# Performance work log

Hardware: AMD Instinct MI355X
Metric: run time of the kernel (lower is better)

Reference implementation:

```python
import jax, jax.numpy as jnp
import numpy as np

STOCH = 32; DETER = 512; OBS = 64; ACT = 8; HID = 512
B = 1024; T = 64
MIN_STD = 0.1; UPD_BIAS = -1.0; LN_EPS = 1e-3


def _ln(x, g, b):
    # LayerNorm(eps=0.001), biased variance as in torch
    m = jnp.mean(x, axis=-1, keepdims=True)
    v = jnp.mean((x - m) ** 2, axis=-1, keepdims=True)
    return (x - m) / jnp.sqrt(v + LN_EPS) * g + b


def setup_inputs() -> dict:
    key = jax.random.key(0)
    ks = jax.random.split(key, 12)
    def rn(k, shape, scale=0.05):
        return jax.random.normal(k, shape, jnp.float32) * scale
    return {
        "obs": jax.random.normal(ks[0], (B, T, OBS), jnp.float32),
        "action": jax.random.normal(ks[1], (B, T, ACT), jnp.float32),
        "is_first": jax.random.randint(ks[2], (B, T), 0, 2, jnp.int32),
        # prior_in: Linear(stoch+act -> hidden, no bias) + LN
        "W_pi": rn(ks[3], (STOCH + ACT, HID)), "g_pi": jnp.ones(HID), "b_pi": jnp.zeros(HID),
        # GRUCell: Linear(hidden+deter -> 3*deter, no bias) + LN
        "W_gru": rn(ks[4], (HID + DETER, 3 * DETER)), "g_gru": jnp.ones(3 * DETER), "b_gru": jnp.zeros(3 * DETER),
        # prior_out: Linear(deter -> hidden, no bias) + LN
        "W_po": rn(ks[5], (DETER, HID)), "g_po": jnp.ones(HID), "b_po": jnp.zeros(HID),
        # prior_stats: Linear(hidden -> 2*stoch)
        "W_ps": rn(ks[6], (HID, 2 * STOCH)), "b_ps": jnp.zeros(2 * STOCH),
        # post_net: Linear(deter+obs -> hidden, no bias) + LN
        "W_pn": rn(ks[7], (DETER + OBS, HID)), "g_pn": jnp.ones(HID), "b_pn": jnp.zeros(HID),
        # post_stats: Linear(hidden -> 2*stoch)
        "W_pt": rn(ks[8], (HID, 2 * STOCH)), "b_pt": jnp.zeros(2 * STOCH),
        # learned initial deterministic state (1, deter)
        "init_deter": rn(ks[9], (1, DETER), 0.1),
    }


def reference(obs, action, is_first,
              W_pi, g_pi, b_pi, W_gru, g_gru, b_gru, W_po, g_po, b_po,
              W_ps, b_ps, W_pn, g_pn, b_pn, W_pt, b_pt, init_deter):
    silu = jax.nn.silu
    Bsz = obs.shape[0]
    # initial_state: deter = tanh(learned), stoch = prior mean at that deter
    d_init = jnp.tanh(init_deter)  # (1, DETER)
    h0 = silu(_ln(d_init @ W_po, g_po, b_po))
    s_init = (h0 @ W_ps + b_ps)[..., :STOCH]  # prior mean
    d_init = jnp.broadcast_to(d_init, (Bsz, DETER))
    s_init = jnp.broadcast_to(s_init, (Bsz, STOCH))

    def step(carry, inp):
        deter, stoch = carry
        obs_t, act_t, first_t = inp  # (B,OBS),(B,ACT),(B,)
        m = (first_t > 0)[:, None]
        deter = jnp.where(m, d_init, deter)
        stoch = jnp.where(m, s_init, stoch)
        act_t = jnp.where(m, 0.0, act_t)
        # prior / img step
        x = silu(_ln(jnp.concatenate([stoch, act_t], -1) @ W_pi, g_pi, b_pi))
        gates = _ln(jnp.concatenate([x, deter], -1) @ W_gru, g_gru, b_gru)
        r, c, u = jnp.split(gates, 3, -1)
        r = jax.nn.sigmoid(r)
        u = jax.nn.sigmoid(u + UPD_BIAS)
        cand = silu(r * c)
        deter_n = u * cand + (1.0 - u) * deter
        hp = silu(_ln(deter_n @ W_po, g_po, b_po))
        ps = hp @ W_ps + b_ps
        p_mean, p_raw = jnp.split(ps, 2, -1)
        p_std = jax.nn.softplus(p_raw) + MIN_STD
        # posterior
        hq = silu(_ln(jnp.concatenate([deter_n, obs_t], -1) @ W_pn, g_pn, b_pn))
        qs = hq @ W_pt + b_pt
        q_mean, q_raw = jnp.split(qs, 2, -1)
        q_std = jax.nn.softplus(q_raw) + MIN_STD
        stoch_n = q_mean  # deterministic (mode) rollout for reproducibility
        out = jnp.concatenate([q_mean, q_std, stoch_n, p_mean, p_std, deter_n], -1)
        return (deter_n, stoch_n), out

    xs = (jnp.swapaxes(obs, 0, 1), jnp.swapaxes(action, 0, 1), jnp.swapaxes(is_first, 0, 1))
    _, outs = jax.lax.scan(step, (d_init, s_init), xs)  # (T,B,5*STOCH+DETER)
    return jnp.swapaxes(outs, 0, 1)  # (B,T,672)
```

## Files before the change

### kernel.cpp

```cpp
#include <hip/hip_runtime.h>
#include <hip/hip_bf16.h>
#include <math.h>

#define BB 1024
#define TT 64
#define OBSN 64
#define ACTN 8
#define STOCHN 32
#define DETERN 512
#define HIDN 512
#define G3N 1536
#define CATPI 40
#define OUTC 672
#define LNEPS 1e-3f
#define MINSTD 0.1f
#define UPDBIAS -1.0f

typedef __attribute__((ext_vector_type(8))) short short8;
typedef __attribute__((ext_vector_type(4))) float f32x4;

__device__ __forceinline__ float sigmoidf_(float x) { return 1.f / (1.f + expf(-x)); }
__device__ __forceinline__ float siluf_(float x) { return x / (1.f + expf(-x)); }
__device__ __forceinline__ float softplusf_(float x) { return (x > 20.f) ? x : log1pf(expf(x)); }

__device__ __forceinline__ float b2f(short u) {
    unsigned x = ((unsigned)(unsigned short)u) << 16;
    return __builtin_bit_cast(float, x);
}
__device__ __forceinline__ short f2b(float f) {
    __hip_bfloat16 h = __float2bfloat16(f);
    return __builtin_bit_cast(short, h);
}

__device__ __forceinline__ f32x4 mfma16(short8 a, short8 b, f32x4 c) {
    return __builtin_amdgcn_mfma_f32_16x16x32_bf16(a, b, c, 0, 0, 0);
}

__device__ __forceinline__ void gload_lds16(const void* g, void* l) {
    __builtin_amdgcn_global_load_lds((const __attribute__((address_space(1))) void*)g,
                                     (__attribute__((address_space(3))) void*)l, 16, 0, 0);
}

__device__ __forceinline__ void wred2(float& a, float& b) {
#pragma unroll
    for (int off = 32; off; off >>= 1) {
        a += __shfl_xor(a, off);
        b += __shfl_xor(b, off);
    }
}

__device__ __forceinline__ short8 frag_ld(const short* base, int row, int ks, int lk) {
    int slot = (ks * 4 + lk) ^ (row & 7);
    return *(const short8*)((const char*)base + row * 1024 + (slot << 4));
}
__device__ __forceinline__ short8 frag_ld64(const short* base, int row, int ks, int lk) {
    int slot = ((ks * 4 + lk) ^ (row & 7)) & 7;
    return *(const short8*)((const char*)base + row * 128 + (slot << 4));
}

template <int NFC, int AMT>
__device__ __forceinline__ void stage_tile(const __hip_bfloat16* A0, int ld0, int K0, const __hip_bfloat16* A1,
                                           int ld1, const __hip_bfloat16* Wt, int ldW, int wn0, int cm0, int k0,
                                           char* smA, char* smB) {
    int tid = threadIdx.x, wid = tid >> 6, lane = tid & 63;
    int rseg = lane >> 3, slot = lane & 7;
    const __hip_bfloat16* Ab;
    int ldA, kloc;
    if (k0 < K0) {
        Ab = A0; ldA = ld0; kloc = k0;
    } else {
        Ab = A1; ldA = ld1; kloc = k0 - K0;
    }
#pragma unroll
    for (int i = 0; i < AMT; ++i) {
        int seg = wid * AMT + i;
        int row = seg * 8 + rseg;
        int kk = kloc + ((slot ^ (row & 7)) << 3);
        gload_lds16(Ab + (size_t)(cm0 + row) * ldA + kk, smA + seg * 1024);
    }
#pragma unroll
    for (int i = 0; i < NFC; ++i) {
        int seg = wid * NFC + i;
        int row = seg * 8 + rseg;
        int kk = k0 + ((slot ^ (row & 7)) << 3);
        gload_lds16(Wt + (size_t)(wn0 + row) * ldW + kk, smB + seg * 1024);
    }
}

template <int NFC, int AMT>
__device__ __forceinline__ void compute_tile(const char* smA, const char* smB, f32x4 (&acc)[AMT][NFC]) {
    int lane = threadIdx.x & 63, wid = threadIdx.x >> 6;
    int wr = wid >> 1, wc = wid & 1;
#pragma unroll
    for (int ks = 0; ks < 2; ++ks) {
        short8 af[AMT], bfr[NFC];
        int kslot = ks * 4 + (lane >> 4);
#pragma unroll
        for (int m = 0; m < AMT; ++m) {
            int row = wr * (16 * AMT) + m * 16 + (lane & 15);
            af[m] = *(const short8*)(smA + row * 128 + ((kslot ^ (row & 7)) << 4));
        }
#pragma unroll
        for (int n = 0; n < NFC; ++n) {
            int row = wc * (16 * NFC) + n * 16 + (lane & 15);
            bfr[n] = *(const short8*)(smB + row * 128 + ((kslot ^ (row & 7)) << 4));
        }
#pragma unroll
        for (int m = 0; m < AMT; ++m)
#pragma unroll
            for (int n = 0; n < NFC; ++n) acc[m][n] = mfma16(af[m], bfr[n], acc[m][n]);
    }
}

template <int NFC, int AMT>
__device__ __forceinline__ void gemm_tile_db(const __hip_bfloat16* A0, int ld0, int K0, const __hip_bfloat16* A1,
                                             int ld1, const __hip_bfloat16* Wt, int ldW, int wn0, float* C, int ldc,
                                             int cm0, int cn0, int nK, char* smem) {
    char* smA[2] = {smem, smem + AMT * 4096};
    char* smB[2] = {smem + 2 * AMT * 4096, smem + 2 * AMT * 4096 + NFC * 4096};
    f32x4 acc[AMT][NFC] = {};
    stage_tile<NFC, AMT>(A0, ld0, K0, A1, ld1, Wt, ldW, wn0, cm0, 0, smA[0], smB[0]);
    for (int kt = 0; kt < nK; ++kt) {
        if (kt + 1 < nK) {
            stage_tile<NFC, AMT>(A0, ld0, K0, A1, ld1, Wt, ldW, wn0, cm0, (kt + 1) * 64, smA[(kt + 1) & 1],
                                 smB[(kt + 1) & 1]);
            constexpr int NL = NFC + AMT;
            if constexpr (NL == 5) asm volatile("s_waitcnt vmcnt(5)" ::: "memory");
            else if constexpr (NL == 4) asm volatile("s_waitcnt vmcnt(4)" ::: "memory");
            else asm volatile("s_waitcnt vmcnt(3)" ::: "memory");
        } else {
            asm volatile("s_waitcnt vmcnt(0)" ::: "memory");
        }
        __builtin_amdgcn_s_barrier();
        compute_tile<NFC, AMT>(smA[kt & 1], smB[kt & 1], acc);
        __builtin_amdgcn_s_barrier();
    }
    int lane = threadIdx.x & 63, wid = threadIdx.x >> 6;
    int wr = wid >> 1, wc = wid & 1;
    int r0 = cm0 + wr * (16 * AMT) + ((lane >> 4) << 2);
    int c0 = cn0 + wc * 16 * NFC + (lane & 15);
#pragma unroll
    for (int m = 0; m < AMT; ++m)
#pragma unroll
        for (int n = 0; n < NFC; ++n)
#pragma unroll
            for (int i = 0; i < 4; ++i)
                C[(size_t)(r0 + m * 16 + i) * ldc + c0 + n * 16] = acc[m][n][i];
}

__global__ __launch_bounds__(256) void k_gemm_gru(const __hip_bfloat16* __restrict__ xbf,
                                                  const __hip_bfloat16* __restrict__ dbf,
                                                  const __hip_bfloat16* __restrict__ WgT,
                                                  float* __restrict__ gates) {
    __shared__ __align__(16) char smem[32768];
    int bm = blockIdx.x & 31, bn = blockIdx.x >> 5;
    gemm_tile_db<3, 1>(xbf, 512, 512, dbf, 512, WgT, 1024, bn * 96, gates, G3N, bm * 32, bn * 96, 16, smem);
}

__global__ __launch_bounds__(256) void k_update(int t, const float* __restrict__ gates,
                                                const float* __restrict__ g_gru, const float* __restrict__ b_gru,
                                                float* __restrict__ deter, __hip_bfloat16* __restrict__ dbf,
                                                float* __restrict__ out) {
    const int tid = threadIdx.x;
    const int prow = tid >> 6, l = tid & 63;
    const int gr = blockIdx.x * 4 + prow;
    const int j0 = l * 8;
    const float* gp = gates + (size_t)gr * G3N;
    float g0[8], g1[8], g2[8];
    float s = 0.f, q = 0.f;
#pragma unroll
    for (int e = 0; e < 8; e += 4) {
        f32x4 a = *(const f32x4*)(gp + j0 + e);
        f32x4 b = *(const f32x4*)(gp + 512 + j0 + e);
        f32x4 c = *(const f32x4*)(gp + 1024 + j0 + e);
#pragma unroll
        for (int u = 0; u < 4; ++u) {
            g0[e + u] = a[u];
            g1[e + u] = b[u];
            g2[e + u] = c[u];
            s += a[u] + b[u] + c[u];
            q += a[u] * a[u] + b[u] * b[u] + c[u] * c[u];
        }
    }
    wred2(s, q);
    float m = s * (1.f / 1536.f), iv = rsqrtf(q * (1.f / 1536.f) - m * m + LNEPS);
    float dn[8];
    float* dp = deter + (size_t)gr * 512 + j0;
#pragma unroll
    for (int e = 0; e < 8; e += 4) {
        f32x4 dv = *(const f32x4*)(dp + e);
#pragma unroll
        for (int u = 0; u < 4; ++u) {
            int col = j0 + e + u;
            float rv = sigmoidf_((g0[e + u] - m) * iv * g_gru[col] + b_gru[col]);
            float cv = (g1[e + u] - m) * iv * g_gru[512 + col] + b_gru[512 + col];
            float uv = sigmoidf_((g2[e + u] - m) * iv * g_gru[1024 + col] + b_gru[1024 + col] + UPDBIAS);
            dn[e + u] = uv * siluf_(rv * cv) + (1.f - uv) * dv[u];
        }
    }
    size_t ob = ((size_t)gr * TT + t) * OUTC + 160 + j0;
    short8 h;
#pragma unroll
    for (int e = 0; e < 8; e += 4) {
        *(f32x4*)(dp + e) = *(const f32x4*)&dn[e];
        *(f32x4*)(out + ob + e) = *(const f32x4*)&dn[e];
    }
#pragma unroll
    for (int u = 0; u < 8; ++u) h[u] = f2b(dn[u]);
    *(short8*)(dbf + (size_t)gr * 512 + j0) = h;
}

__global__ __launch_bounds__(256) void k_gemm_hq(int t, const __hip_bfloat16* __restrict__ dbf,
                                                 const __hip_bfloat16* __restrict__ obsbf,
                                                 const __hip_bfloat16* __restrict__ WpnT,
                                                 float* __restrict__ hq_raw) {
    __shared__ __align__(16) char smem[24576];
    int bm = blockIdx.x & 31, bn = blockIdx.x >> 5;
    gemm_tile_db<2, 1>(dbf, 512, 512, obsbf + (size_t)t * OBSN, TT * OBSN, WpnT, 576, bn * 64, hq_raw, 512,
                       bm * 32, bn * 64, 9, smem);
}

__global__ __launch_bounds__(256) void k_finish(int t, const float* __restrict__ hq_raw,
                                                const float* __restrict__ g_pn, const float* __restrict__ b_pn,
                                                const __hip_bfloat16* __restrict__ WptT,
                                                const float* __restrict__ b_pt, const int* __restrict__ isf,
                                                const float* __restrict__ action, const float* __restrict__ dinit,
                                                const float* __restrict__ sinit, float* __restrict__ deter,
                                                __hip_bfloat16* __restrict__ dbf,
                                                const __hip_bfloat16* __restrict__ Wpibf,
                                                const float* __restrict__ g_pi, const float* __restrict__ b_pi,
                                                __hip_bfloat16* __restrict__ xbf, float* __restrict__ out) {
    __shared__ float hql[4][512];
    __shared__ float a_ls[4][40];
    const int wid = threadIdx.x >> 6, l = threadIdx.x & 63;
    const int gr = blockIdx.x * 4 + wid;
    const int j0 = l * 8;
    const float* hr = hq_raw + (size_t)gr * 512;
    float h[8];
    *(f32x4*)&h[0] = *(const f32x4*)(hr + j0);
    *(f32x4*)&h[4] = *(const f32x4*)(hr + j0 + 4);
    float s = 0.f, q = 0.f;
#pragma unroll
    for (int e = 0; e < 8; ++e) {
        s += h[e];
        q += h[e] * h[e];
    }
    wred2(s, q);
    float m = s * (1.f / 512.f), iv = rsqrtf(q * (1.f / 512.f) - m * m + LNEPS);
#pragma unroll
    for (int e = 0; e < 8; ++e) h[e] = siluf_((h[e] - m) * iv * g_pn[j0 + e] + b_pn[j0 + e]);
    *(f32x4*)&hql[wid][j0] = *(const f32x4*)&h[0];
    *(f32x4*)&hql[wid][j0 + 4] = *(const f32x4*)&h[4];
    __syncthreads();
    float acc = b_pt[l];
    const __hip_bfloat16* wr = WptT + (size_t)l * 512;
    const float* hq = hql[wid];
#pragma unroll 4
    for (int k0 = 0; k0 < 512; k0 += 8) {
        short8 w = *(const short8*)(wr + k0);
        f32x4 a0 = *(const f32x4*)(hq + k0);
        f32x4 a1 = *(const f32x4*)(hq + k0 + 4);
#pragma unroll
        for (int e = 0; e < 4; ++e) {
            acc += b2f(w[e]) * a0[e];
            acc += b2f(w[4 + e]) * a1[e];
        }
    }
    size_t ob = ((size_t)gr * TT + t) * OUTC;
    if (l < 32) {
        out[ob + l] = acc;
        out[ob + 64 + l] = acc;
    } else {
        out[ob + 32 + (l - 32)] = softplusf_(acc) + MINSTD;
    }
    if (t + 1 >= TT) return;
    int f1 = isf[(size_t)gr * TT + t + 1] > 0;
    if (l < 32)
        a_ls[wid][l] = f1 ? sinit[l] : acc;
    else if (l < 40)
        a_ls[wid][l] = f1 ? 0.f : action[((size_t)gr * TT + t + 1) * ACTN + (l - 32)];
    if (f1) {
        f32x4 d0 = *(const f32x4*)(dinit + j0);
        f32x4 d1 = *(const f32x4*)(dinit + j0 + 4);
        *(f32x4*)(deter + (size_t)gr * 512 + j0) = d0;
        *(f32x4*)(deter + (size_t)gr * 512 + j0 + 4) = d1;
        short8 db;
#pragma unroll
        for (int e = 0; e < 4; ++e) {
            db[e] = f2b(d0[e]);
            db[4 + e] = f2b(d1[e]);
        }
        *(short8*)(dbf + (size_t)gr * 512 + j0) = db;
    }
    __syncthreads();
    float o[8] = {};
    const float* a_s = a_ls[wid];
    for (int k = 0; k < CATPI; ++k) {
        float a = a_s[k];
        short8 w = *(const short8*)(Wpibf + k * 512 + j0);
#pragma unroll
        for (int e = 0; e < 8; ++e) o[e] += a * b2f(w[e]);
    }
    float s2 = 0.f, q2 = 0.f;
#pragma unroll
    for (int e = 0; e < 8; ++e) {
        s2 += o[e];
        q2 += o[e] * o[e];
    }
    wred2(s2, q2);
    float m2 = s2 * (1.f / 512.f), iv2 = rsqrtf(q2 * (1.f / 512.f) - m2 * m2 + LNEPS);
    short8 xo;
#pragma unroll
    for (int e = 0; e < 8; ++e) xo[e] = f2b(siluf_((o[e] - m2) * iv2 * g_pi[j0 + e] + b_pi[j0 + e]));
    *(short8*)(xbf + (size_t)gr * 512 + j0) = xo;
}

__global__ __launch_bounds__(512) void k_post_p(const float* __restrict__ outr,
                                                const __hip_bfloat16* __restrict__ WpoT,
                                                const float* __restrict__ g_po, const float* __restrict__ b_po,
                                                const __hip_bfloat16* __restrict__ WpsT,
                                                const float* __restrict__ b_ps, float* __restrict__ out) {
    __shared__ short Abuf[64 * 512];
    __shared__ __align__(16) short Wbuf[512 * 64];
    __shared__ float red[8 * 64 * 2];
    __shared__ float redc[64 * 2];
    const int tid = threadIdx.x, wid = tid >> 6, lane = tid & 63, lr = lane & 15, lk = lane >> 4;
    const int base = blockIdx.x * 64;
    const int c0 = wid * 64 + lr;

#pragma unroll
    for (int it = 0; it < 8; ++it) {
        int idx = it * 512 + tid;
        int row = idx >> 6, slot = idx & 63;
        int k = (slot ^ (row & 7)) << 3;
        const float* src = outr + ((size_t)(base + row) * OUTC + 160 + k);
        f32x4 a = *(const f32x4*)src;
        f32x4 bb = *(const f32x4*)(src + 4);
        short8 v;
#pragma unroll
        for (int e = 0; e < 4; ++e) {
            v[e] = f2b(a[e]);
            v[4 + e] = f2b(bb[e]);
        }
        *(short8*)((char*)Abuf + idx * 16) = v;
    }
    auto stageW = [&](int ck) {
#pragma unroll
        for (int i = 0; i < 8; ++i) {
            int seg = wid * 8 + i;
            int row = seg * 8 + (lane >> 3);
            int kk = ck * 64 + (((lane & 7) ^ (row & 7)) << 3);
            gload_lds16(WpoT + (size_t)row * 512 + kk, (char*)Wbuf + seg * 1024);
        }
    };
    __syncthreads();
    f32x4 acc[4][4] = {};
    for (int ck = 0; ck < 8; ++ck) {
        stageW(ck);
        asm volatile("s_waitcnt vmcnt(0)" ::: "memory");
        __builtin_amdgcn_s_barrier();
#pragma unroll
        for (int ks = 0; ks < 2; ++ks) {
            short8 af[4];
#pragma unroll
            for (int rt = 0; rt < 4; ++rt) af[rt] = frag_ld(Abuf, rt * 16 + lr, ck * 2 + ks, lk);
#pragma unroll
            for (int f = 0; f < 4; ++f) {
                short8 bf = frag_ld64(Wbuf, c0 + f * 16, ks, lk);
#pragma unroll
                for (int rt = 0; rt < 4; ++rt) acc[rt][f] = mfma16(af[rt], bf, acc[rt][f]);
            }
        }
        __builtin_amdgcn_s_barrier();
    }
#pragma unroll
    for (int qq = 0; qq < 8; ++qq) {
        int sI = qq * 512 + tid;
        int row = sI >> 6, slot = sI & 63;
        int k = (slot ^ (row & 7)) << 3;
        gload_lds16(WpsT + (size_t)row * 512 + k, (char*)Abuf + (qq * 512 + wid * 64) * 16);
    }
    {
        float s[4][4], q[4][4];
#pragma unroll
        for (int rt = 0; rt < 4; ++rt)
#pragma unroll
            for (int i = 0; i < 4; ++i) {
                float ss = 0.f, qq2 = 0.f;
#pragma unroll
                for (int f = 0; f < 4; ++f) {
                    float v = acc[rt][f][i];
                    ss += v;
                    qq2 += v * v;
                }
                s[rt][i] = ss;
                q[rt][i] = qq2;
            }
#pragma unroll
        for (int msk = 1; msk <= 8; msk <<= 1)
#pragma unroll
            for (int rt = 0; rt < 4; ++rt)
#pragma unroll
                for (int i = 0; i < 4; ++i) {
                    s[rt][i] += __shfl_xor(s[rt][i], msk);
                    q[rt][i] += __shfl_xor(q[rt][i], msk);
                }
        if (lr == 0)
#pragma unroll
            for (int rt = 0; rt < 4; ++rt)
#pragma unroll
                for (int i = 0; i < 4; ++i) {
                    int row = rt * 16 + lk * 4 + i;
                    red[(wid * 64 + row) * 2 + 0] = s[rt][i];
                    red[(wid * 64 + row) * 2 + 1] = q[rt][i];
                }
        __syncthreads();
        if (tid < 128) {
            int row = tid >> 1, v = tid & 1;
            float a = 0.f;
#pragma unroll
            for (int w = 0; w < 8; ++w) a += red[(w * 64 + row) * 2 + v];
            redc[row * 2 + v] = a;
        }
        __syncthreads();
#pragma unroll
        for (int rt = 0; rt < 4; ++rt)
#pragma unroll
            for (int i = 0; i < 4; ++i) {
                int row = rt * 16 + lk * 4 + i;
                float mm = redc[row * 2] * (1.f / 512.f);
                float vv = redc[row * 2 + 1] * (1.f / 512.f) - mm * mm;
                float ivv = rsqrtf(vv + LNEPS);
#pragma unroll
                for (int f = 0; f < 4; ++f) {
                    int col = c0 + f * 16;
                    float v = siluf_((acc[rt][f][i] - mm) * ivv * g_po[col] + b_po[col]);
                    *(short*)((char*)Wbuf + row * 1024 +
                              ((((col >> 3) ^ (row & 7)) << 4) | ((col & 7) << 1))) = f2b(v);
                }
            }
    }
    asm volatile("s_waitcnt vmcnt(0)" ::: "memory");
    __syncthreads();
    if (wid < 4) {
        int col = wid * 16 + lr;
        f32x4 ap[4] = {};
#pragma unroll 2
        for (int ks = 0; ks < 16; ++ks) {
            short8 bfr = frag_ld(Abuf, col, ks, lk);
#pragma unroll
            for (int rt = 0; rt < 4; ++rt) {
                short8 a = frag_ld(Wbuf, rt * 16 + lr, ks, lk);
                ap[rt] = mfma16(a, bfr, ap[rt]);
            }
        }
        float bias = b_ps[col];
#pragma unroll
        for (int rt = 0; rt < 4; ++rt)
#pragma unroll
            for (int i = 0; i < 4; ++i) {
                int gidx = base + rt * 16 + lk * 4 + i;
                float v = ap[rt][i] + bias;
                if (col < 32)
                    out[(size_t)gidx * OUTC + 96 + col] = v;
                else
                    out[(size_t)gidx * OUTC + 128 + (col - 32)] = softplusf_(v) + MINSTD;
            }
    }
}

__global__ __launch_bounds__(256) void k_prior0(const int* __restrict__ isf, const float* __restrict__ action,
                                                const float* __restrict__ dinit, const float* __restrict__ sinit,
                                                const __hip_bfloat16* __restrict__ Wpibf,
                                                const float* __restrict__ g_pi, const float* __restrict__ b_pi,
                                                float* __restrict__ deter0, __hip_bfloat16* __restrict__ dbf,
                                                __hip_bfloat16* __restrict__ xbf) {
    __shared__ float a_ls[4][40];
    const int wid = threadIdx.x >> 6, l = threadIdx.x & 63;
    const int gr = blockIdx.x * 4 + wid;
    const int j0 = l * 8;
    int f0 = isf[(size_t)gr * TT] > 0;
    if (l < 32)
        a_ls[wid][l] = sinit[l];
    else if (l < 40)
        a_ls[wid][l] = f0 ? 0.f : action[(size_t)gr * TT * ACTN + (l - 32)];
    f32x4 d0 = *(const f32x4*)(dinit + j0);
    f32x4 d1 = *(const f32x4*)(dinit + j0 + 4);
    *(f32x4*)(deter0 + (size_t)gr * 512 + j0) = d0;
    *(f32x4*)(deter0 + (size_t)gr * 512 + j0 + 4) = d1;
    short8 db;
#pragma unroll
    for (int e = 0; e < 4; ++e) {
        db[e] = f2b(d0[e]);
        db[4 + e] = f2b(d1[e]);
    }
    *(short8*)(dbf + (size_t)gr * 512 + j0) = db;
    __syncthreads();
    float o[8] = {};
    const float* a_s = a_ls[wid];
    for (int k = 0; k < CATPI; ++k) {
        float a = a_s[k];
        short8 w = *(const short8*)(Wpibf + k * 512 + j0);
#pragma unroll
        for (int e = 0; e < 8; ++e) o[e] += a * b2f(w[e]);
    }
    float s2 = 0.f, q2 = 0.f;
#pragma unroll
    for (int e = 0; e < 8; ++e) {
        s2 += o[e];
        q2 += o[e] * o[e];
    }
    wred2(s2, q2);
    float m2 = s2 * (1.f / 512.f), iv2 = rsqrtf(q2 * (1.f / 512.f) - m2 * m2 + LNEPS);
    short8 xo;
#pragma unroll
    for (int e = 0; e < 8; ++e) xo[e] = f2b(siluf_((o[e] - m2) * iv2 * g_pi[j0 + e] + b_pi[j0 + e]));
    *(short8*)(xbf + (size_t)gr * 512 + j0) = xo;
}

template <int NV>
__device__ __forceinline__ void breduce(float* v, float* red, int nwaves) {
    __syncthreads();
#pragma unroll
    for (int off = 32; off > 0; off >>= 1)
#pragma unroll
        for (int q = 0; q < NV; ++q) v[q] += __shfl_down(v[q], off);
    int lane = threadIdx.x & 63, w = threadIdx.x >> 6;
    if (lane == 0)
        for (int q = 0; q < NV; ++q) red[w * NV + q] = v[q];
    __syncthreads();
    if ((int)threadIdx.x < NV) {
        float s = 0.f;
        for (int ww = 0; ww < nwaves; ++ww) s += red[ww * NV + threadIdx.x];
        red[nwaves * NV + threadIdx.x] = s;
    }
    __syncthreads();
#pragma unroll
    for (int q = 0; q < NV; ++q) v[q] = red[nwaves * NV + q];
}

__global__ __launch_bounds__(512) void k_init(const float* __restrict__ init_deter, const float* __restrict__ W_po,
                                              const float* __restrict__ g_po, const float* __restrict__ b_po,
                                              const float* __restrict__ W_ps, const float* __restrict__ b_ps,
                                              float* __restrict__ dinit, float* __restrict__ sinit) {
    __shared__ float d_s[512], h_s[512], red[40];
    int tid = threadIdx.x;
    float dv = tanhf(init_deter[tid]);
    d_s[tid] = dv;
    dinit[tid] = dv;
    __syncthreads();
    float acc = 0.f;
    for (int k = 0; k < 512; ++k) acc += d_s[k] * W_po[k * 512 + tid];
    float v[2] = {acc, acc * acc};
    breduce<2>(v, red, 8);
    float m = v[0] / 512.f, va = v[1] / 512.f - m * m, iv = rsqrtf(va + LNEPS);
    h_s[tid] = siluf_((acc - m) * iv * g_po[tid] + b_po[tid]);
    __syncthreads();
    if (tid < 32) {
        float s = b_ps[tid];
        for (int k = 0; k < 512; ++k) s += h_s[k] * W_ps[k * 64 + tid];
        sinit[tid] = s;
    }
}

__global__ __launch_bounds__(256) void k_transpose_bf(const float* __restrict__ src,
                                                      __hip_bfloat16* __restrict__ dst, int K, int N) {
    __shared__ float tle[32][33];
    int nTK = K >> 5;
    int k0 = (blockIdx.x % nTK) * 32;
    int n0 = (blockIdx.x / nTK) * 32;
    int tx = threadIdx.x & 31, ty = threadIdx.x >> 5;
#pragma unroll
    for (int i = 0; i < 4; ++i) tle[ty + i * 8][tx] = src[(size_t)(k0 + ty + i * 8) * N + n0 + tx];
    __syncthreads();
#pragma unroll
    for (int i = 0; i < 4; ++i)
        dst[(size_t)(n0 + ty + i * 8) * K + k0 + tx] = __float2bfloat16(tle[tx][ty + i * 8]);
}

__global__ __launch_bounds__(256) void k_cvt_bf(const float* __restrict__ src, __hip_bfloat16* __restrict__ dst,
                                                int n) {
    for (int i = blockIdx.x * 256 + threadIdx.x; i < n; i += gridDim.x * 256) dst[i] = __float2bfloat16(src[i]);
}

extern "C" void kernel_launch(void* const* d_in, const int* in_sizes, int n_in, void* d_out, int out_size, void* d_ws,
                              size_t ws_size, hipStream_t stream) {
    const float* obs = (const float*)d_in[0];
    const float* action = (const float*)d_in[1];
    const int* is_first = (const int*)d_in[2];
    const float* W_pi = (const float*)d_in[3];
    const float* g_pi = (const float*)d_in[4];
    const float* b_pi = (const float*)d_in[5];
    const float* W_gru = (const float*)d_in[6];
    const float* g_gru = (const float*)d_in[7];
    const float* b_gru = (const float*)d_in[8];
    const float* W_po = (const float*)d_in[9];
    const float* g_po = (const float*)d_in[10];
    const float* b_po = (const float*)d_in[11];
    const float* W_ps = (const float*)d_in[12];
    const float* b_ps = (const float*)d_in[13];
    const float* W_pn = (const float*)d_in[14];
    const float* g_pn = (const float*)d_in[15];
    const float* b_pn = (const float*)d_in[16];
    const float* W_pt = (const float*)d_in[17];
    const float* b_pt = (const float*)d_in[18];
    const float* init_deter = (const float*)d_in[19];
    float* out = (float*)d_out;

    char* p = (char*)d_ws;
    auto alloc = [&](size_t bytes) {
        char* r = p;
        p += (bytes + 255) & ~(size_t)255;
        return r;
    };
    float* gates = (float*)alloc((size_t)BB * G3N * 4);
    float* deter = (float*)alloc((size_t)BB * 512 * 4);
    float* hq_raw = (float*)alloc((size_t)BB * 512 * 4);
    float* dinit = (float*)alloc(512 * 4);
    float* sinit = (float*)alloc(64 * 4);
    __hip_bfloat16* xbf = (__hip_bfloat16*)alloc((size_t)BB * 512 * 2);
    __hip_bfloat16* dbf = (__hip_bfloat16*)alloc((size_t)BB * 512 * 2);
    __hip_bfloat16* obsbf = (__hip_bfloat16*)alloc((size_t)BB * TT * OBSN * 2);
    __hip_bfloat16* WgT = (__hip_bfloat16*)alloc((size_t)G3N * 1024 * 2);
    __hip_bfloat16* WpoT = (__hip_bfloat16*)alloc((size_t)512 * 512 * 2);
    __hip_bfloat16* WpnT = (__hip_bfloat16*)alloc((size_t)512 * 576 * 2);
    __hip_bfloat16* WpsT = (__hip_bfloat16*)alloc((size_t)64 * 512 * 2);
    __hip_bfloat16* WptT = (__hip_bfloat16*)alloc((size_t)64 * 512 * 2);
    __hip_bfloat16* Wpibf = (__hip_bfloat16*)alloc((size_t)CATPI * 512 * 2);

    k_transpose_bf<<<(1024 / 32) * (G3N / 32), 256, 0, stream>>>(W_gru, WgT, 1024, G3N);
    k_transpose_bf<<<(512 / 32) * (512 / 32), 256, 0, stream>>>(W_po, WpoT, 512, 512);
    k_transpose_bf<<<(576 / 32) * (512 / 32), 256, 0, stream>>>(W_pn, WpnT, 576, 512);
    k_transpose_bf<<<(512 / 32) * (64 / 32), 256, 0, stream>>>(W_ps, WpsT, 512, 64);
    k_transpose_bf<<<(512 / 32) * (64 / 32), 256, 0, stream>>>(W_pt, WptT, 512, 64);
    k_cvt_bf<<<80, 256, 0, stream>>>(W_pi, Wpibf, CATPI * 512);
    k_cvt_bf<<<2048, 256, 0, stream>>>(obs, obsbf, BB * TT * OBSN);
    k_init<<<1, 512, 0, stream>>>(init_deter, W_po, g_po, b_po, W_ps, b_ps, dinit, sinit);
    k_prior0<<<256, 256, 0, stream>>>(is_first, action, dinit, sinit, Wpibf, g_pi, b_pi, deter, dbf, xbf);

    for (int t = 0; t < TT; ++t) {
        k_gemm_gru<<<512, 256, 0, stream>>>(xbf, dbf, WgT, gates);
        k_update<<<256, 256, 0, stream>>>(t, gates, g_gru, b_gru, deter, dbf, out);
        k_gemm_hq<<<256, 256, 0, stream>>>(t, dbf, obsbf, WpnT, hq_raw);
        k_finish<<<256, 256, 0, stream>>>(t, hq_raw, g_pn, b_pn, WptT, b_pt, is_first, action, dinit, sinit, deter,
                                          dbf, Wpibf, g_pi, b_pi, xbf, out);
    }
    k_post_p<<<BB * TT / 64, 512, 0, stream>>>(out, WpoT, g_po, b_po, WpsT, b_ps, out);
}
```

Measured before the change: 2.307 ms.

## Split-K the per-step GRU and posterior GEMMs to double grid parallelism

Both per-timestep GEMMs are split along K into two halves, each written to its own partial-sum buffer, which doubles the number of workgroups launched (1024 and 512 instead of 512 and 256). The consumer kernels k_update and k_finish now add the two partials before the LayerNorm. The aim is to fill more of the GPU's compute units, since the original grids are small relative to the device. The cost is extra fp32 partial traffic, twice the gates and hq_raw buffers, and an extra load per element in the consumers.

After: 2.437 ms. 5.6% more time.

```diff
diff --git a/kernel.cpp b/kernel.cpp
--- a/kernel.cpp
+++ b/kernel.cpp
@@ -153,8 +153,10 @@
                                                   const __hip_bfloat16* __restrict__ WgT,
                                                   float* __restrict__ gates) {
     __shared__ __align__(16) char smem[32768];
-    int bm = blockIdx.x & 31, bn = blockIdx.x >> 5;
-    gemm_tile_db<3, 1>(xbf, 512, 512, dbf, 512, WgT, 1024, bn * 96, gates, G3N, bm * 32, bn * 96, 16, smem);
+    int bm = blockIdx.x & 31, bn = (blockIdx.x >> 5) & 15, kh = blockIdx.x >> 9;
+    const __hip_bfloat16* A = kh ? dbf : xbf;
+    gemm_tile_db<3, 1>(A, 512, 512, A, 512, WgT + kh * 512, 1024, bn * 96,
+                       gates + (size_t)kh * BB * G3N, G3N, bm * 32, bn * 96, 8, smem);
 }
 
 __global__ __launch_bounds__(256) void k_update(int t, const float* __restrict__ gates,
@@ -165,21 +167,26 @@
     const int prow = tid >> 6, l = tid & 63;
     const int gr = blockIdx.x * 4 + prow;
     const int j0 = l * 8;
-    const float* gp = gates + (size_t)gr * G3N;
+    const float* gp0 = gates + (size_t)gr * G3N;
+    const float* gp1 = gates + (size_t)BB * G3N + (size_t)gr * G3N;
     float g0[8], g1[8], g2[8];
     float s = 0.f, q = 0.f;
 #pragma unroll
     for (int e = 0; e < 8; e += 4) {
-        f32x4 a = *(const f32x4*)(gp + j0 + e);
-        f32x4 b = *(const f32x4*)(gp + 512 + j0 + e);
-        f32x4 c = *(const f32x4*)(gp + 1024 + j0 + e);
+        f32x4 a0 = *(const f32x4*)(gp0 + j0 + e);
+        f32x4 b0 = *(const f32x4*)(gp0 + 512 + j0 + e);
+        f32x4 c0 = *(const f32x4*)(gp0 + 1024 + j0 + e);
+        f32x4 a1 = *(const f32x4*)(gp1 + j0 + e);
+        f32x4 b1 = *(const f32x4*)(gp1 + 512 + j0 + e);
+        f32x4 c1 = *(const f32x4*)(gp1 + 1024 + j0 + e);
 #pragma unroll
         for (int u = 0; u < 4; ++u) {
-            g0[e + u] = a[u];
-            g1[e + u] = b[u];
-            g2[e + u] = c[u];
-            s += a[u] + b[u] + c[u];
-            q += a[u] * a[u] + b[u] * b[u] + c[u] * c[u];
+            float a = a0[u] + a1[u], b = b0[u] + b1[u], c = c0[u] + c1[u];
+            g0[e + u] = a;
+            g1[e + u] = b;
+            g2[e + u] = c;
+            s += a + b + c;
+            q += a * a + b * b + c * c;
         }
     }
     wred2(s, q);
@@ -215,9 +222,13 @@
                                                  const __hip_bfloat16* __restrict__ WpnT,
                                                  float* __restrict__ hq_raw) {
     __shared__ __align__(16) char smem[24576];
-    int bm = blockIdx.x & 31, bn = blockIdx.x >> 5;
-    gemm_tile_db<2, 1>(dbf, 512, 512, obsbf + (size_t)t * OBSN, TT * OBSN, WpnT, 576, bn * 64, hq_raw, 512,
-                       bm * 32, bn * 64, 9, smem);
+    int bm = blockIdx.x & 31, bn = (blockIdx.x >> 5) & 7, kh = blockIdx.x >> 8;
+    if (kh == 0) {
+        gemm_tile_db<2, 1>(dbf, 512, 512, dbf, 512, WpnT, 576, bn * 64, hq_raw, 512, bm * 32, bn * 64, 5, smem);
+    } else {
+        gemm_tile_db<2, 1>(dbf + 320, 512, 192, obsbf + (size_t)t * OBSN, TT * OBSN, WpnT + 320, 576, bn * 64,
+                           hq_raw + (size_t)BB * 512, 512, bm * 32, bn * 64, 4, smem);
+    }
 }
 
 __global__ __launch_bounds__(256) void k_finish(int t, const float* __restrict__ hq_raw,
@@ -235,10 +246,20 @@
     const int wid = threadIdx.x >> 6, l = threadIdx.x & 63;
     const int gr = blockIdx.x * 4 + wid;
     const int j0 = l * 8;
-    const float* hr = hq_raw + (size_t)gr * 512;
+    const float* hr0 = hq_raw + (size_t)gr * 512;
+    const float* hr1 = hq_raw + (size_t)BB * 512 + (size_t)gr * 512;
     float h[8];
-    *(f32x4*)&h[0] = *(const f32x4*)(hr + j0);
-    *(f32x4*)&h[4] = *(const f32x4*)(hr + j0 + 4);
+    {
+        f32x4 a0 = *(const f32x4*)(hr0 + j0);
+        f32x4 a1 = *(const f32x4*)(hr0 + j0 + 4);
+        f32x4 b0 = *(const f32x4*)(hr1 + j0);
+        f32x4 b1 = *(const f32x4*)(hr1 + j0 + 4);
+#pragma unroll
+        for (int e = 0; e < 4; ++e) {
+            h[e] = a0[e] + b0[e];
+            h[4 + e] = a1[e] + b1[e];
+        }
+    }
     float s = 0.f, q = 0.f;
 #pragma unroll
     for (int e = 0; e < 8; ++e) {
@@ -613,9 +634,9 @@
         p += (bytes + 255) & ~(size_t)255;
         return r;
     };
-    float* gates = (float*)alloc((size_t)BB * G3N * 4);
+    float* gates = (float*)alloc((size_t)2 * BB * G3N * 4);
     float* deter = (float*)alloc((size_t)BB * 512 * 4);
-    float* hq_raw = (float*)alloc((size_t)BB * 512 * 4);
+    float* hq_raw = (float*)alloc((size_t)2 * BB * 512 * 4);
     float* dinit = (float*)alloc(512 * 4);
     float* sinit = (float*)alloc(64 * 4);
     __hip_bfloat16* xbf = (__hip_bfloat16*)alloc((size_t)BB * 512 * 2);
@@ -639,9 +660,9 @@
     k_prior0<<<256, 256, 0, stream>>>(is_first, action, dinit, sinit, Wpibf, g_pi, b_pi, deter, dbf, xbf);
 
     for (int t = 0; t < TT; ++t) {
-        k_gemm_gru<<<512, 256, 0, stream>>>(xbf, dbf, WgT, gates);
+        k_gemm_gru<<<1024, 256, 0, stream>>>(xbf, dbf, WgT, gates);
         k_update<<<256, 256, 0, stream>>>(t, gates, g_gru, b_gru, deter, dbf, out);
-        k_gemm_hq<<<256, 256, 0, stream>>>(t, dbf, obsbf, WpnT, hq_raw);
+        k_gemm_hq<<<512, 256, 0, stream>>>(t, dbf, obsbf, WpnT, hq_raw);
         k_finish<<<256, 256, 0, stream>>>(t, hq_raw, g_pn, b_pn, WptT, b_pt, is_first, action, dinit, sinit, deter,
                                           dbf, Wpibf, g_pi, b_pi, xbf, out);
     }
```
